# Kernel optimization log

Measured on AMD Instinct MI355X. Metric: run time of the kernel, lower is better.

Reference implementation:

```python
import jax, jax.numpy as jnp
import numpy as np

EPS = 1e-5  # torch BatchNorm1d default eps

N_NODES = 100000
N_EDGES = 1250000
N_GRAPHS = 512
F_IN = 16
HID = 64


def _bn(x, w, b):
    # track_running_stats=False, momentum=None -> always batch statistics (biased var)
    m = jnp.mean(x, axis=0)
    v = jnp.var(x, axis=0)
    return (x - m) * jax.lax.rsqrt(v + EPS) * w + b


def _prelu(x, a):
    return jnp.where(x >= 0, x, a * x)


def _gcn_conv(x, W, b, src, dst, n):
    # PyG GCNConv: h = x W; add self loops; sym-norm by deg^-1/2 on target degrees
    h = x @ W  # [N, out]
    ones = jnp.ones(src.shape[0], x.dtype)
    deg = jax.ops.segment_sum(ones, dst, num_segments=n) + 1.0  # +1 self loop
    dis = jax.lax.rsqrt(deg)  # deg >= 1 so finite
    norm = (dis[src] * dis[dst])[:, None]  # [E,1]
    agg = jax.ops.segment_sum(h[src] * norm, dst, num_segments=n)
    # self-loop contribution: norm = dis[i]*dis[i]
    return agg + h * (dis * dis)[:, None] + b


def setup_inputs() -> dict:
    key = jax.random.key(0)
    ks = jax.random.split(key, 12)
    x = jax.random.normal(ks[0], (N_NODES, F_IN), dtype=jnp.float32)
    edge_index = jax.random.randint(ks[1], (2, N_EDGES), 0, N_NODES, dtype=jnp.int32)
    # evenly spaced graph ids so every segment is non-empty (global_max_pool)
    batch = ((jnp.arange(N_NODES, dtype=jnp.int32) * N_GRAPHS) // N_NODES).astype(jnp.int32)
    s = 0.1
    W1 = jax.random.normal(ks[2], (F_IN, HID), jnp.float32) * s
    b1 = jnp.zeros((HID,), jnp.float32)
    W2 = jax.random.normal(ks[3], (HID, HID), jnp.float32) * s
    b2 = jnp.zeros((HID,), jnp.float32)
    lw1 = jax.random.normal(ks[4], (HID, HID), jnp.float32) * s
    lb1 = jnp.zeros((HID,), jnp.float32)
    lw2 = jax.random.normal(ks[5], (HID, 1), jnp.float32) * s
    lb2 = jnp.zeros((1,), jnp.float32)
    bn1_w = jnp.ones((HID,), jnp.float32); bn1_b = jnp.zeros((HID,), jnp.float32)
    bn2_w = jnp.ones((HID,), jnp.float32); bn2_b = jnp.zeros((HID,), jnp.float32)
    bn3_w = jnp.ones((HID,), jnp.float32); bn3_b = jnp.zeros((HID,), jnp.float32)
    bn4_w = jnp.ones((1,), jnp.float32); bn4_b = jnp.zeros((1,), jnp.float32)
    a1 = jnp.full((1,), 0.25, jnp.float32)
    a2 = jnp.full((1,), 0.25, jnp.float32)
    a3 = jnp.full((1,), 0.25, jnp.float32)
    a4 = jnp.full((1,), 0.25, jnp.float32)
    return {"x": x, "edge_index": edge_index, "batch": batch,
            "W1": W1, "b1": b1, "W2": W2, "b2": b2,
            "bn1_w": bn1_w, "bn1_b": bn1_b, "bn2_w": bn2_w, "bn2_b": bn2_b,
            "bn3_w": bn3_w, "bn3_b": bn3_b, "bn4_w": bn4_w, "bn4_b": bn4_b,
            "lw1": lw1, "lb1": lb1, "lw2": lw2, "lb2": lb2,
            "a1": a1, "a2": a2, "a3": a3, "a4": a4}


def reference(x, edge_index, batch, W1, b1, W2, b2,
              bn1_w, bn1_b, bn2_w, bn2_b, bn3_w, bn3_b, bn4_w, bn4_b,
              lw1, lb1, lw2, lb2, a1, a2, a3, a4):
    src, dst = edge_index[0], edge_index[1]
    n = x.shape[0]
    h = _gcn_conv(x, W1, b1, src, dst, n)
    h = _prelu(_bn(h, bn1_w, bn1_b), a1)
    h = _gcn_conv(h, W2, b2, src, dst, n)
    h = _prelu(_bn(h, bn2_w, bn2_b), a2)
    g = jax.ops.segment_max(h, batch, num_segments=N_GRAPHS)  # global_max_pool
    g = _prelu(_bn(g @ lw1 + lb1, bn3_w, bn3_b), a3)
    g = _prelu(_bn(g @ lw2 + lb2, bn4_w, bn4_b), a4)
    return g
```

## Files before the change

kernel.cpp:

```cpp
#include <hip/hip_runtime.h>
#include <hip/hip_bf16.h>

#define N_NODES 100000
#define N_EDGES 1250000
#define N_GRAPHS 512
#define F_IN 16
#define HID 64
#define EPS 1e-5f

#define K_B 1563
#define B_H 250
#define EPB 5000
#define M_SC (K_B * B_H)

typedef unsigned int uint;

__device__ __forceinline__ uint f2bf(float f) {
    uint u = __float_as_uint(f);
    return (u + 0x7fffu + ((u >> 16) & 1u)) >> 16;
}
__device__ __forceinline__ uint pack2(float lo, float hi) {
    return f2bf(lo) | (f2bf(hi) << 16);
}
__device__ __forceinline__ void unpack8(float* o, uint4 v) {
    o[0] = __uint_as_float(v.x << 16); o[1] = __uint_as_float(v.x & 0xffff0000u);
    o[2] = __uint_as_float(v.y << 16); o[3] = __uint_as_float(v.y & 0xffff0000u);
    o[4] = __uint_as_float(v.z << 16); o[5] = __uint_as_float(v.z & 0xffff0000u);
    o[6] = __uint_as_float(v.w << 16); o[7] = __uint_as_float(v.w & 0xffff0000u);
}
__device__ __forceinline__ void accum8(float* a, uint4 v) {
    a[0] += __uint_as_float(v.x << 16); a[1] += __uint_as_float(v.x & 0xffff0000u);
    a[2] += __uint_as_float(v.y << 16); a[3] += __uint_as_float(v.y & 0xffff0000u);
    a[4] += __uint_as_float(v.z << 16); a[5] += __uint_as_float(v.z & 0xffff0000u);
    a[6] += __uint_as_float(v.w << 16); a[7] += __uint_as_float(v.w & 0xffff0000u);
}


__global__ __launch_bounds__(256) void k_hist(const int4* __restrict__ dst4,
                                              int* __restrict__ hist,
                                              float* __restrict__ statsr) {
    __shared__ int h[K_B];
    int t = threadIdx.x, b = blockIdx.x;
    if (b == 0) {
        for (int i = t; i < 6 * 512; i += 256) statsr[i] = 0.f;
    }
    for (int k = t; k < K_B; k += 256) h[k] = 0;
    __syncthreads();
    const int4* d4 = dst4 + b * (EPB / 4);
    for (int i = t; i < EPB / 4; i += 256) {
        int4 d = d4[i];
        atomicAdd(&h[d.x >> 6], 1);
        atomicAdd(&h[d.y >> 6], 1);
        atomicAdd(&h[d.z >> 6], 1);
        atomicAdd(&h[d.w >> 6], 1);
    }
    __syncthreads();
    for (int k = t; k < K_B; k += 256) hist[k * B_H + b] = h[k];
}

__global__ void k_s1(const int* __restrict__ in, int* __restrict__ out,
                     int* __restrict__ bsum, int n) {
    __shared__ int sh[256];
    int blk = blockIdx.x, t = threadIdx.x;
    int base = blk * 1024 + t * 4;
    int v[4];
#pragma unroll
    for (int j = 0; j < 4; j++) { int i = base + j; v[j] = (i < n) ? in[i] : 0; }
    int tsum = v[0] + v[1] + v[2] + v[3];
    sh[t] = tsum;
    __syncthreads();
    for (int ofs = 1; ofs < 256; ofs <<= 1) {
        int x = (t >= ofs) ? sh[t - ofs] : 0;
        __syncthreads();
        sh[t] += x;
        __syncthreads();
    }
    int run = sh[t] - tsum;
    if (t == 255) bsum[blk] = sh[255];
#pragma unroll
    for (int j = 0; j < 4; j++) { int i = base + j; if (i < n) out[i] = run; run += v[j]; }
}

__global__ void k_s2(int* __restrict__ bsum, int nb) {
    __shared__ int sh[256];
    int t = threadIdx.x;
    int v[4]; int s = 0;
#pragma unroll
    for (int j = 0; j < 4; j++) { int i = t * 4 + j; v[j] = (i < nb) ? bsum[i] : 0; s += v[j]; }
    sh[t] = s;
    __syncthreads();
    for (int ofs = 1; ofs < 256; ofs <<= 1) {
        int x = (t >= ofs) ? sh[t - ofs] : 0;
        __syncthreads();
        sh[t] += x;
        __syncthreads();
    }
    int run = sh[t] - s;
#pragma unroll
    for (int j = 0; j < 4; j++) { int i = t * 4 + j; if (i < nb) bsum[i] = run; run += v[j]; }
}

__global__ __launch_bounds__(256) void k_bucketize(const int4* __restrict__ src4,
        const int4* __restrict__ dst4, const int* __restrict__ ebase,
        const int* __restrict__ bsum, int* __restrict__ ebuck) {
    __shared__ int base[K_B];
    int t = threadIdx.x, b = blockIdx.x;
    for (int k = t; k < K_B; k += 256) {
        int idx = k * B_H + b;
        base[k] = ebase[idx] + bsum[idx >> 10];
    }
    __syncthreads();
    const int4* s4 = src4 + b * (EPB / 4);
    const int4* d4 = dst4 + b * (EPB / 4);
    for (int i = t; i < EPB / 4; i += 256) {
        int4 s = s4[i];
        int4 d = d4[i];
        int p;
        p = atomicAdd(&base[d.x >> 6], 1); ebuck[p] = s.x | ((d.x & 63) << 17);
        p = atomicAdd(&base[d.y >> 6], 1); ebuck[p] = s.y | ((d.y & 63) << 17);
        p = atomicAdd(&base[d.z >> 6], 1); ebuck[p] = s.z | ((d.z & 63) << 17);
        p = atomicAdd(&base[d.w >> 6], 1); ebuck[p] = s.w | ((d.w & 63) << 17);
    }
}

__global__ __launch_bounds__(256) void k_csr(const int* __restrict__ ebase,
        const int* __restrict__ bsum, const int* __restrict__ ebuck,
        int* __restrict__ col, int2* __restrict__ meta, float* __restrict__ dis) {
    int k = blockIdx.x, t = threadIdx.x;
    int i0 = k * B_H;
    int beg = ebase[i0] + bsum[i0 >> 10];
    int end;
    if (k + 1 < K_B) {
        int i1 = i0 + B_H;
        end = ebase[i1] + bsum[i1 >> 10];
    } else {
        end = N_EDGES;
    }
    int m = end - beg;
    __shared__ int eb[2048];
    __shared__ int cnt512[512];
    __shared__ int off512[512];
    __shared__ int sb[512];
    __shared__ int sh[256];
    for (int i = t; i < 512; i += 256) cnt512[i] = 0;
    __syncthreads();
    if (m <= 2048) {
        for (int i = t; i < m; i += 256) {
            int e = ebuck[beg + i];
            eb[i] = e;
            int bin = ((e >> 17) << 3) | ((e & 0x1FFFF) >> 14);
            atomicAdd(&cnt512[bin], 1);
        }
        __syncthreads();
        int v0 = cnt512[2 * t], v1 = cnt512[2 * t + 1];
        int pair = v0 + v1;
        sh[t] = pair;
        __syncthreads();
        for (int ofs = 1; ofs < 256; ofs <<= 1) {
            int x = (t >= ofs) ? sh[t - ofs] : 0;
            __syncthreads();
            sh[t] += x;
            __syncthreads();
        }
        int excl = sh[t] - pair;
        off512[2 * t] = excl;
        off512[2 * t + 1] = excl + v0;
        sb[2 * t] = beg + excl;
        sb[2 * t + 1] = beg + excl + v0;
        __syncthreads();
        if (t < 64) {
            int o0 = off512[t * 8];
            int o1 = (t < 63) ? off512[(t + 1) * 8] : m;
            int node = k * 64 + t;
            if (node < N_NODES) {
                meta[node] = make_int2(beg + o0, o1 - o0);
                dis[node] = rsqrtf((float)(o1 - o0) + 1.0f);
            }
        }
        __syncthreads();
        for (int i = t; i < m; i += 256) {
            int e = eb[i];
            int bin = ((e >> 17) << 3) | ((e & 0x1FFFF) >> 14);
            int pos = atomicAdd(&sb[bin], 1);
            col[pos] = e & 0x1FFFF;
        }
    } else {
        for (int i = t; i < m; i += 256) atomicAdd(&cnt512[ebuck[beg + i] >> 17], 1);
        __syncthreads();
        if (t < 64) {
            int v = cnt512[t];
            int incl = v;
#pragma unroll
            for (int o = 1; o < 64; o <<= 1) { int u = __shfl_up(incl, o); if (t >= o) incl += u; }
            int excl = incl - v;
            int node = k * 64 + t;
            if (node < N_NODES) {
                meta[node] = make_int2(beg + excl, v);
                dis[node] = rsqrtf((float)v + 1.0f);
            }
            sb[t] = beg + excl;
        }
        __syncthreads();
        for (int i = t; i < m; i += 256) {
            int e = ebuck[beg + i];
            int pos = atomicAdd(&sb[e >> 17], 1);
            col[pos] = e & 0x1FFFF;
        }
    }
}


__global__ __launch_bounds__(512) void k_gemm1(const float* __restrict__ x,
        const float* __restrict__ W1, const float* __restrict__ dis,
        ushort* __restrict__ A) {
    __shared__ float Ws[F_IN * HID];
    __shared__ float xs[32 * F_IN];
    int t = threadIdx.x;
    Ws[t] = W1[t];
    Ws[t + 512] = W1[t + 512];
    int n0 = blockIdx.x * 32;
    xs[t] = x[n0 * F_IN + t];
    __syncthreads();
    int f = t & 63, w = t >> 6;
    float Wreg[F_IN];
#pragma unroll
    for (int k = 0; k < F_IN; k++) Wreg[k] = Ws[k * HID + f];
#pragma unroll
    for (int i = 0; i < 4; i++) {
        int nl = w * 4 + i;
        float acc = 0.f;
#pragma unroll
        for (int kq = 0; kq < 4; kq++) {
            const float4 xv = *(const float4*)&xs[nl * F_IN + kq * 4];
            acc = fmaf(xv.x, Wreg[4 * kq + 0], acc);
            acc = fmaf(xv.y, Wreg[4 * kq + 1], acc);
            acc = fmaf(xv.z, Wreg[4 * kq + 2], acc);
            acc = fmaf(xv.w, Wreg[4 * kq + 3], acc);
        }
        int n = n0 + nl;
        A[(size_t)n * HID + f] = (ushort)f2bf(acc * dis[n]);
    }
}

__global__ __launch_bounds__(512) void k_gemm2(const ushort* __restrict__ B,
        const float* __restrict__ s1r, const float* __restrict__ ss1r,
        const float* __restrict__ bnw, const float* __restrict__ bnb,
        const float* __restrict__ alpha, const float* __restrict__ W2,
        const float* __restrict__ dis, ushort* __restrict__ A2) {
    __shared__ float Ws[HID * HID];
    __shared__ float xs[32 * HID];
    __shared__ float scs[64], shsv[64];
    int t = threadIdx.x;
#pragma unroll
    for (int i = 0; i < 8; i++) Ws[i * 512 + t] = W2[i * 512 + t];
    if (t < 64) {
        float s = 0, q = 0;
#pragma unroll
        for (int r = 0; r < 8; r++) { s += s1r[r * 64 + t]; q += ss1r[r * 64 + t]; }
        const float invn = 1.f / N_NODES;
        float m = s * invn;
        float v = q * invn - m * m;
        float sc = bnw[t] * rsqrtf(v + EPS);
        scs[t] = sc;
        shsv[t] = bnb[t] - m * sc;
    }
    __syncthreads();
    int n0 = blockIdx.x * 32;
    float al = alpha[0];
    {
        const uint* Bu = (const uint*)(B + (size_t)n0 * HID);
#pragma unroll
        for (int i = 0; i < 2; i++) {
            int idx = i * 512 + t;
            uint u = Bu[idx];
            int fp = (idx & 31) * 2;
            int row = idx >> 5;
            float lo = __uint_as_float(u << 16) * scs[fp] + shsv[fp];
            float hi = __uint_as_float(u & 0xffff0000u) * scs[fp + 1] + shsv[fp + 1];
            lo = lo >= 0.f ? lo : al * lo;
            hi = hi >= 0.f ? hi : al * hi;
            xs[row * HID + fp] = lo;
            xs[row * HID + fp + 1] = hi;
        }
    }
    __syncthreads();
    int f = t & 63, w = t >> 6;
    float Wreg[HID];
#pragma unroll
    for (int k = 0; k < HID; k++) Wreg[k] = Ws[k * HID + f];
#pragma unroll
    for (int i = 0; i < 4; i++) {
        int nl = w * 4 + i;
        float acc = 0.f;
#pragma unroll
        for (int kq = 0; kq < 16; kq++) {
            const float4 xv = *(const float4*)&xs[nl * HID + kq * 4];
            acc = fmaf(xv.x, Wreg[4 * kq + 0], acc);
            acc = fmaf(xv.y, Wreg[4 * kq + 1], acc);
            acc = fmaf(xv.z, Wreg[4 * kq + 2], acc);
            acc = fmaf(xv.w, Wreg[4 * kq + 3], acc);
        }
        int n = n0 + nl;
        A2[(size_t)n * HID + f] = (ushort)f2bf(acc * dis[n]);
    }
}

__global__ __launch_bounds__(256) void k_agg(const uint4* __restrict__ Asc,
        const float* __restrict__ dis, const int2* __restrict__ meta,
        const int* __restrict__ col, const float* __restrict__ bias,
        uint4* __restrict__ outB, float* __restrict__ sumr,
        float* __restrict__ sumsqr) {
    int t = threadIdx.x;
    int nid = blockIdx.x * 32 + (t >> 3);
    int fq = t & 7;
    int2 mt = meta[nid];
    int beg = mt.x, m = mt.y;
    float acc[8] = {0, 0, 0, 0, 0, 0, 0, 0};
    int j = 0;
    for (; j + 8 <= m; j += 8) {
        int s0 = col[beg + j];
        int s1 = col[beg + j + 1];
        int s2 = col[beg + j + 2];
        int s3 = col[beg + j + 3];
        int s4 = col[beg + j + 4];
        int s5 = col[beg + j + 5];
        int s6 = col[beg + j + 6];
        int s7 = col[beg + j + 7];
        uint4 r0 = Asc[(size_t)s0 * 8 + fq];
        uint4 r1 = Asc[(size_t)s1 * 8 + fq];
        uint4 r2 = Asc[(size_t)s2 * 8 + fq];
        uint4 r3 = Asc[(size_t)s3 * 8 + fq];
        uint4 r4 = Asc[(size_t)s4 * 8 + fq];
        uint4 r5 = Asc[(size_t)s5 * 8 + fq];
        uint4 r6 = Asc[(size_t)s6 * 8 + fq];
        uint4 r7 = Asc[(size_t)s7 * 8 + fq];
        accum8(acc, r0); accum8(acc, r1); accum8(acc, r2); accum8(acc, r3);
        accum8(acc, r4); accum8(acc, r5); accum8(acc, r6); accum8(acc, r7);
    }
    for (; j + 2 <= m; j += 2) {
        int s0 = col[beg + j];
        int s1 = col[beg + j + 1];
        uint4 r0 = Asc[(size_t)s0 * 8 + fq];
        uint4 r1 = Asc[(size_t)s1 * 8 + fq];
        accum8(acc, r0); accum8(acc, r1);
    }
    if (j < m) {
        int s = col[beg + j];
        accum8(acc, Asc[(size_t)s * 8 + fq]);
    }
    accum8(acc, Asc[(size_t)nid * 8 + fq]);
    float dn = dis[nid];
    float4 b0 = ((const float4*)bias)[fq * 2];
    float4 b1 = ((const float4*)bias)[fq * 2 + 1];
    float o[8];
    o[0] = b0.x + dn * acc[0]; o[1] = b0.y + dn * acc[1];
    o[2] = b0.z + dn * acc[2]; o[3] = b0.w + dn * acc[3];
    o[4] = b1.x + dn * acc[4]; o[5] = b1.y + dn * acc[5];
    o[6] = b1.z + dn * acc[6]; o[7] = b1.w + dn * acc[7];
    uint4 ov;
    ov.x = pack2(o[0], o[1]); ov.y = pack2(o[2], o[3]);
    ov.z = pack2(o[4], o[5]); ov.w = pack2(o[6], o[7]);
    outB[(size_t)nid * 8 + fq] = ov;

    float sq[8];
#pragma unroll
    for (int i = 0; i < 8; i++) sq[i] = o[i] * o[i];
#pragma unroll
    for (int ofs = 8; ofs <= 32; ofs <<= 1) {
#pragma unroll
        for (int i = 0; i < 8; i++) {
            o[i] += __shfl_xor(o[i], ofs);
            sq[i] += __shfl_xor(sq[i], ofs);
        }
    }
    __shared__ float ps[4][64], pq[4][64];
    int w = t >> 6, lane = t & 63;
    if (lane < 8) {
#pragma unroll
        for (int i = 0; i < 8; i++) {
            ps[w][lane * 8 + i] = o[i];
            pq[w][lane * 8 + i] = sq[i];
        }
    }
    __syncthreads();
    if (t < 64) {
        float a = ps[0][t] + ps[1][t] + ps[2][t] + ps[3][t];
        float b = pq[0][t] + pq[1][t] + pq[2][t] + pq[3][t];
        int rep = (blockIdx.x & 7) * 64;
        atomicAdd(&sumr[rep + t], a);
        atomicAdd(&sumsqr[rep + t], b);
    }
}

__global__ __launch_bounds__(256) void k_pool(const uint4* __restrict__ a,
        const float* __restrict__ s2r, const float* __restrict__ ss2r,
        const float* __restrict__ bnw, const float* __restrict__ bnb,
        const float* __restrict__ alpha, const float* __restrict__ lw1,
        const float* __restrict__ lb1, float* __restrict__ th,
        float* __restrict__ s3r, float* __restrict__ ss3r) {
    __shared__ float scs[64], shsv[64];
    __shared__ float sm[2048];
    __shared__ float gr[64];
    int gi = blockIdx.x;
    int t = threadIdx.x, rg = t >> 3, fq = t & 7;
    if (t < 64) {
        float s = 0, q = 0;
#pragma unroll
        for (int r = 0; r < 8; r++) { s += s2r[r * 64 + t]; q += ss2r[r * 64 + t]; }
        const float invn = 1.f / N_NODES;
        float m = s * invn;
        float v = q * invn - m * m;
        float sc = bnw[t] * rsqrtf(v + EPS);
        scs[t] = sc;
        shsv[t] = bnb[t] - m * sc;
    }
    __syncthreads();
    int lo = (gi * N_NODES + N_GRAPHS - 1) / N_GRAPHS;
    int hi = ((gi + 1) * N_NODES + N_GRAPHS - 1) / N_GRAPHS;
    float al = alpha[0];
    float sc[8], sh[8];
#pragma unroll
    for (int i = 0; i < 8; i++) { sc[i] = scs[fq * 8 + i]; sh[i] = shsv[fq * 8 + i]; }
    float mx[8];
#pragma unroll
    for (int i = 0; i < 8; i++) mx[i] = -INFINITY;
    for (int r = lo + rg; r < hi; r += 32) {
        float o[8];
        unpack8(o, a[(size_t)r * 8 + fq]);
#pragma unroll
        for (int i = 0; i < 8; i++) {
            float v = o[i] * sc[i] + sh[i];
            v = v >= 0.f ? v : al * v;
            mx[i] = fmaxf(mx[i], v);
        }
    }
#pragma unroll
    for (int i = 0; i < 8; i++) sm[rg * 64 + fq * 8 + i] = mx[i];
    __syncthreads();
    if (t < 64) {
        float m = sm[t];
#pragma unroll
        for (int i = 1; i < 32; i++) m = fmaxf(m, sm[i * 64 + t]);
        gr[t] = m;
    }
    __syncthreads();
    if (t < 64) {
        float acc = lb1[t];
#pragma unroll
        for (int k = 0; k < 64; k++) acc = fmaf(gr[k], lw1[k * 64 + t], acc);
        th[gi * 64 + t] = acc;
        int rep = (gi & 7) * 64;
        atomicAdd(&s3r[rep + t], acc);
        atomicAdd(&ss3r[rep + t], acc * acc);
    }
}

__global__ __launch_bounds__(512) void k_head(const float* __restrict__ th,
        const float* __restrict__ s3r, const float* __restrict__ ss3r,
        const float* __restrict__ bn3w, const float* __restrict__ bn3b,
        const float* __restrict__ a3, const float* __restrict__ lw2,
        const float* __restrict__ lb2, const float* __restrict__ bn4w,
        const float* __restrict__ bn4b, const float* __restrict__ a4,
        float* __restrict__ out) {
    int t = threadIdx.x, w = t >> 6, lane = t & 63;
    __shared__ float t2s[N_GRAPHS];
    __shared__ float rs[8], rq[8];
    const float invn = 1.f / N_GRAPHS;
    float s = 0, q = 0;
#pragma unroll
    for (int r = 0; r < 8; r++) { s += s3r[r * 64 + lane]; q += ss3r[r * 64 + lane]; }
    float m3 = s * invn;
    float v3 = q * invn - m3 * m3;
    float sc3 = bn3w[lane] * rsqrtf(v3 + EPS);
    float sh3 = bn3b[lane] - m3 * sc3;
    float al3 = a3[0];
    float wv = lw2[lane];
    float lb = lb2[0];
    for (int r = w; r < N_GRAPHS; r += 8) {
        float xv = th[r * 64 + lane] * sc3 + sh3;
        xv = xv >= 0.f ? xv : al3 * xv;
        float p = xv * wv;
#pragma unroll
        for (int o = 32; o > 0; o >>= 1) p += __shfl_xor(p, o);
        if (lane == 0) t2s[r] = p + lb;
    }
    __syncthreads();
    float tv = t2s[t];
    float ps = tv, pq = tv * tv;
#pragma unroll
    for (int o = 32; o > 0; o >>= 1) { ps += __shfl_xor(ps, o); pq += __shfl_xor(pq, o); }
    if (lane == 0) { rs[w] = ps; rq[w] = pq; }
    __syncthreads();
    float S = 0, Q = 0;
#pragma unroll
    for (int i = 0; i < 8; i++) { S += rs[i]; Q += rq[i]; }
    float m4 = S * invn;
    float v4 = Q * invn - m4 * m4;
    float sc4 = bn4w[0] * rsqrtf(v4 + EPS);
    float xb = (tv - m4) * sc4 + bn4b[0];
    float al4 = a4[0];
    out[t] = xb >= 0.f ? xb : al4 * xb;
}

extern "C" void kernel_launch(void* const* d_in, const int* in_sizes, int n_in,
                              void* d_out, int out_size, void* d_ws, size_t ws_size,
                              hipStream_t stream) {
    const float* x   = (const float*)d_in[0];
    const int*   ei  = (const int*)d_in[1];
    const int4*  src4 = (const int4*)ei;
    const int4*  dst4 = (const int4*)(ei + N_EDGES);
    const float* W1  = (const float*)d_in[3];
    const float* b1  = (const float*)d_in[4];
    const float* W2  = (const float*)d_in[5];
    const float* b2  = (const float*)d_in[6];
    const float* bn1w = (const float*)d_in[7];
    const float* bn1b = (const float*)d_in[8];
    const float* bn2w = (const float*)d_in[9];
    const float* bn2b = (const float*)d_in[10];
    const float* bn3w = (const float*)d_in[11];
    const float* bn3b = (const float*)d_in[12];
    const float* bn4w = (const float*)d_in[13];
    const float* bn4b = (const float*)d_in[14];
    const float* lw1  = (const float*)d_in[15];
    const float* lb1  = (const float*)d_in[16];
    const float* lw2  = (const float*)d_in[17];
    const float* lb2  = (const float*)d_in[18];
    const float* a1   = (const float*)d_in[19];
    const float* a2   = (const float*)d_in[20];
    const float* a3   = (const float*)d_in[21];
    const float* a4   = (const float*)d_in[22];
    float* out = (float*)d_out;

    char* p = (char*)d_ws;
    auto carve = [&](size_t bytes) -> void* {
        void* r = (void*)p;
        p += (bytes + 255) & ~(size_t)255;
        return r;
    };
    int*    hist = (int*)carve((size_t)M_SC * 4);
    int*    ebase = (int*)carve((size_t)M_SC * 4);
    int*    ebuck = (int*)carve((size_t)N_EDGES * 4);
    int*    col  = (int*)carve((size_t)N_EDGES * 4);
    float*  dis  = (float*)carve((size_t)N_NODES * 4);
    int2*   meta = (int2*)carve((size_t)N_NODES * 8);
    int*    bsum = (int*)carve(4096);
    ushort* A    = (ushort*)carve((size_t)N_NODES * HID * 2);
    ushort* B    = (ushort*)carve((size_t)N_NODES * HID * 2);
    float*  th   = (float*)carve((size_t)N_GRAPHS * HID * 4);
    float*  statsr = (float*)carve(6 * 512 * 4);
    float* s1r = statsr,          *ss1r = statsr + 512;
    float* s2r = statsr + 1024,   *ss2r = statsr + 1536;
    float* s3r = statsr + 2048,   *ss3r = statsr + 2560;

    const int SC_BLKS = (M_SC + 1023) / 1024;

    k_hist<<<B_H, 256, 0, stream>>>(dst4, hist, statsr);
    k_s1<<<SC_BLKS, 256, 0, stream>>>(hist, ebase, bsum, M_SC);
    k_s2<<<1, 256, 0, stream>>>(bsum, SC_BLKS);
    k_bucketize<<<B_H, 256, 0, stream>>>(src4, dst4, ebase, bsum, ebuck);
    k_csr<<<K_B, 256, 0, stream>>>(ebase, bsum, ebuck, col, meta, dis);

    const int NB32 = N_NODES / 32;
    k_gemm1<<<NB32, 512, 0, stream>>>(x, W1, dis, A);
    k_agg<<<NB32, 256, 0, stream>>>((const uint4*)A, dis, meta, col, b1, (uint4*)B,
                                    s1r, ss1r);
    k_gemm2<<<NB32, 512, 0, stream>>>(B, s1r, ss1r, bn1w, bn1b, a1, W2, dis, A);
    k_agg<<<NB32, 256, 0, stream>>>((const uint4*)A, dis, meta, col, b2, (uint4*)B,
                                    s2r, ss2r);
    k_pool<<<N_GRAPHS, 256, 0, stream>>>((const uint4*)B, s2r, ss2r, bn2w, bn2b, a2,
                                         lw1, lb1, th, s3r, ss3r);
    k_head<<<1, 512, 0, stream>>>(th, s3r, ss3r, bn3w, bn3b, a3, lw2, lb2,
                                  bn4w, bn4b, a4, out);
}
```

Measured before the change: 179.1 us.

## Store node features in feature-chunk-major layout and aggregate one chunk at a time

Node feature buffers change from row-major [N,64] bf16 to eight chunk-major planes of [N,8] bf16. The aggregation kernel now gives each node two threads and loops over the eight chunks, so each gather pass touches a 1.6MB plane that fits in cache better. The GEMM, pool and BN-stat code are updated to match. The cost is that the col indices are reread eight times per node, and each chunk adds shuffle reductions, two block syncs and atomics, with 16-byte gathers shrunk to 8 bytes.

Result: slower. 254.6 us (+42.1%).

```diff
diff --git a/kernel.cpp b/kernel.cpp
--- a/kernel.cpp
+++ b/kernel.cpp
@@ -28,11 +28,9 @@
     o[4] = __uint_as_float(v.z << 16); o[5] = __uint_as_float(v.z & 0xffff0000u);
     o[6] = __uint_as_float(v.w << 16); o[7] = __uint_as_float(v.w & 0xffff0000u);
 }
-__device__ __forceinline__ void accum8(float* a, uint4 v) {
+__device__ __forceinline__ void accum4(float* a, uint2 v) {
     a[0] += __uint_as_float(v.x << 16); a[1] += __uint_as_float(v.x & 0xffff0000u);
     a[2] += __uint_as_float(v.y << 16); a[3] += __uint_as_float(v.y & 0xffff0000u);
-    a[4] += __uint_as_float(v.z << 16); a[5] += __uint_as_float(v.z & 0xffff0000u);
-    a[6] += __uint_as_float(v.w << 16); a[7] += __uint_as_float(v.w & 0xffff0000u);
 }
 
 
@@ -225,6 +223,7 @@
     float Wreg[F_IN];
 #pragma unroll
     for (int k = 0; k < F_IN; k++) Wreg[k] = Ws[k * HID + f];
+    size_t fbase = (size_t)(f >> 3) * N_NODES * 8 + (f & 7);
 #pragma unroll
     for (int i = 0; i < 4; i++) {
         int nl = w * 4 + i;
@@ -238,7 +237,7 @@
             acc = fmaf(xv.w, Wreg[4 * kq + 3], acc);
         }
         int n = n0 + nl;
-        A[(size_t)n * HID + f] = (ushort)f2bf(acc * dis[n]);
+        A[fbase + (size_t)n * 8] = (ushort)f2bf(acc * dis[n]);
     }
 }
 
@@ -268,19 +267,19 @@
     int n0 = blockIdx.x * 32;
     float al = alpha[0];
     {
-        const uint* Bu = (const uint*)(B + (size_t)n0 * HID);
+        const uint* Bu = (const uint*)B;
 #pragma unroll
         for (int i = 0; i < 2; i++) {
-            int idx = i * 512 + t;
-            uint u = Bu[idx];
-            int fp = (idx & 31) * 2;
-            int row = idx >> 5;
+            int id = i * 512 + t;
+            int c = id >> 7, r = (id >> 2) & 31, jj = id & 3;
+            uint u = Bu[((size_t)c * N_NODES + n0 + r) * 4 + jj];
+            int fp = c * 8 + jj * 2;
             float lo = __uint_as_float(u << 16) * scs[fp] + shsv[fp];
             float hi = __uint_as_float(u & 0xffff0000u) * scs[fp + 1] + shsv[fp + 1];
             lo = lo >= 0.f ? lo : al * lo;
             hi = hi >= 0.f ? hi : al * hi;
-            xs[row * HID + fp] = lo;
-            xs[row * HID + fp + 1] = hi;
+            xs[r * HID + fp] = lo;
+            xs[r * HID + fp + 1] = hi;
         }
     }
     __syncthreads();
@@ -288,6 +287,7 @@
     float Wreg[HID];
 #pragma unroll
     for (int k = 0; k < HID; k++) Wreg[k] = Ws[k * HID + f];
+    size_t fbase = (size_t)(f >> 3) * N_NODES * 8 + (f & 7);
 #pragma unroll
     for (int i = 0; i < 4; i++) {
         int nl = w * 4 + i;
@@ -301,94 +301,78 @@
             acc = fmaf(xv.w, Wreg[4 * kq + 3], acc);
         }
         int n = n0 + nl;
-        A2[(size_t)n * HID + f] = (ushort)f2bf(acc * dis[n]);
-    }
-}
-
-__global__ __launch_bounds__(256) void k_agg(const uint4* __restrict__ Asc,
+        A2[fbase + (size_t)n * 8] = (ushort)f2bf(acc * dis[n]);
+    }
+}
+
+__global__ __launch_bounds__(256) void k_agg(const uint2* __restrict__ Asc,
         const float* __restrict__ dis, const int2* __restrict__ meta,
         const int* __restrict__ col, const float* __restrict__ bias,
-        uint4* __restrict__ outB, float* __restrict__ sumr,
+        uint2* __restrict__ outB, float* __restrict__ sumr,
         float* __restrict__ sumsqr) {
     int t = threadIdx.x;
-    int nid = blockIdx.x * 32 + (t >> 3);
-    int fq = t & 7;
-    int2 mt = meta[nid];
-    int beg = mt.x, m = mt.y;
-    float acc[8] = {0, 0, 0, 0, 0, 0, 0, 0};
-    int j = 0;
-    for (; j + 8 <= m; j += 8) {
-        int s0 = col[beg + j];
-        int s1 = col[beg + j + 1];
-        int s2 = col[beg + j + 2];
-        int s3 = col[beg + j + 3];
-        int s4 = col[beg + j + 4];
-        int s5 = col[beg + j + 5];
-        int s6 = col[beg + j + 6];
-        int s7 = col[beg + j + 7];
-        uint4 r0 = Asc[(size_t)s0 * 8 + fq];
-        uint4 r1 = Asc[(size_t)s1 * 8 + fq];
-        uint4 r2 = Asc[(size_t)s2 * 8 + fq];
-        uint4 r3 = Asc[(size_t)s3 * 8 + fq];
-        uint4 r4 = Asc[(size_t)s4 * 8 + fq];
-        uint4 r5 = Asc[(size_t)s5 * 8 + fq];
-        uint4 r6 = Asc[(size_t)s6 * 8 + fq];
-        uint4 r7 = Asc[(size_t)s7 * 8 + fq];
-        accum8(acc, r0); accum8(acc, r1); accum8(acc, r2); accum8(acc, r3);
-        accum8(acc, r4); accum8(acc, r5); accum8(acc, r6); accum8(acc, r7);
-    }
-    for (; j + 2 <= m; j += 2) {
-        int s0 = col[beg + j];
-        int s1 = col[beg + j + 1];
-        uint4 r0 = Asc[(size_t)s0 * 8 + fq];
-        uint4 r1 = Asc[(size_t)s1 * 8 + fq];
-        accum8(acc, r0); accum8(acc, r1);
-    }
-    if (j < m) {
-        int s = col[beg + j];
-        accum8(acc, Asc[(size_t)s * 8 + fq]);
-    }
-    accum8(acc, Asc[(size_t)nid * 8 + fq]);
-    float dn = dis[nid];
-    float4 b0 = ((const float4*)bias)[fq * 2];
-    float4 b1 = ((const float4*)bias)[fq * 2 + 1];
-    float o[8];
-    o[0] = b0.x + dn * acc[0]; o[1] = b0.y + dn * acc[1];
-    o[2] = b0.z + dn * acc[2]; o[3] = b0.w + dn * acc[3];
-    o[4] = b1.x + dn * acc[4]; o[5] = b1.y + dn * acc[5];
-    o[6] = b1.z + dn * acc[6]; o[7] = b1.w + dn * acc[7];
-    uint4 ov;
-    ov.x = pack2(o[0], o[1]); ov.y = pack2(o[2], o[3]);
-    ov.z = pack2(o[4], o[5]); ov.w = pack2(o[6], o[7]);
-    outB[(size_t)nid * 8 + fq] = ov;
-
-    float sq[8];
-#pragma unroll
-    for (int i = 0; i < 8; i++) sq[i] = o[i] * o[i];
-#pragma unroll
-    for (int ofs = 8; ofs <= 32; ofs <<= 1) {
-#pragma unroll
-        for (int i = 0; i < 8; i++) {
-            o[i] += __shfl_xor(o[i], ofs);
-            sq[i] += __shfl_xor(sq[i], ofs);
-        }
-    }
-    __shared__ float ps[4][64], pq[4][64];
-    int w = t >> 6, lane = t & 63;
-    if (lane < 8) {
-#pragma unroll
-        for (int i = 0; i < 8; i++) {
-            ps[w][lane * 8 + i] = o[i];
-            pq[w][lane * 8 + i] = sq[i];
-        }
-    }
-    __syncthreads();
-    if (t < 64) {
-        float a = ps[0][t] + ps[1][t] + ps[2][t] + ps[3][t];
-        float b = pq[0][t] + pq[1][t] + pq[2][t] + pq[3][t];
-        int rep = (blockIdx.x & 7) * 64;
-        atomicAdd(&sumr[rep + t], a);
-        atomicAdd(&sumsqr[rep + t], b);
+    int nid = blockIdx.x * 128 + (t >> 1);
+    int l = t & 1;
+    bool act = nid < N_NODES;
+    int beg = 0, m = 0; float dn = 0.f;
+    if (act) { int2 mt = meta[nid]; beg = mt.x; m = mt.y; dn = dis[nid]; }
+    int w = t >> 6;
+    int rep = (blockIdx.x & 7) * 64;
+    __shared__ float ps[4][8], pq[4][8];
+    for (int c = 0; c < 8; ++c) {
+        const uint2* __restrict__ Ac = Asc + (size_t)c * N_NODES * 2;
+        float acc[4] = {0.f, 0.f, 0.f, 0.f};
+        int j = 0;
+        for (; j + 4 <= m; j += 4) {
+            int s0 = col[beg + j];
+            int s1 = col[beg + j + 1];
+            int s2 = col[beg + j + 2];
+            int s3 = col[beg + j + 3];
+            uint2 r0 = Ac[(size_t)s0 * 2 + l];
+            uint2 r1 = Ac[(size_t)s1 * 2 + l];
+            uint2 r2 = Ac[(size_t)s2 * 2 + l];
+            uint2 r3 = Ac[(size_t)s3 * 2 + l];
+            accum4(acc, r0); accum4(acc, r1); accum4(acc, r2); accum4(acc, r3);
+        }
+        for (; j < m; ++j) {
+            int s = col[beg + j];
+            accum4(acc, Ac[(size_t)s * 2 + l]);
+        }
+        if (act) accum4(acc, Ac[(size_t)nid * 2 + l]);
+        float4 bv = ((const float4*)bias)[c * 2 + l];
+        float o[4];
+        o[0] = bv.x + dn * acc[0]; o[1] = bv.y + dn * acc[1];
+        o[2] = bv.z + dn * acc[2]; o[3] = bv.w + dn * acc[3];
+        if (act) {
+            uint2 ov;
+            ov.x = pack2(o[0], o[1]); ov.y = pack2(o[2], o[3]);
+            outB[((size_t)c * N_NODES + nid) * 2 + l] = ov;
+        } else {
+            o[0] = o[1] = o[2] = o[3] = 0.f;
+        }
+        float sq[4];
+#pragma unroll
+        for (int i = 0; i < 4; i++) sq[i] = o[i] * o[i];
+#pragma unroll
+        for (int ofs = 2; ofs <= 32; ofs <<= 1) {
+#pragma unroll
+            for (int i = 0; i < 4; i++) {
+                o[i] += __shfl_xor(o[i], ofs);
+                sq[i] += __shfl_xor(sq[i], ofs);
+            }
+        }
+        if ((t & 63) < 2) {
+#pragma unroll
+            for (int i = 0; i < 4; i++) { ps[w][l * 4 + i] = o[i]; pq[w][l * 4 + i] = sq[i]; }
+        }
+        __syncthreads();
+        if (t < 8) {
+            float a = ps[0][t] + ps[1][t] + ps[2][t] + ps[3][t];
+            float b = pq[0][t] + pq[1][t] + pq[2][t] + pq[3][t];
+            atomicAdd(&sumr[rep + c * 8 + t], a);
+            atomicAdd(&sumsqr[rep + c * 8 + t], b);
+        }
+        __syncthreads();
     }
 }
 
@@ -424,9 +408,10 @@
     float mx[8];
 #pragma unroll
     for (int i = 0; i < 8; i++) mx[i] = -INFINITY;
+    const uint4* ac = a + (size_t)fq * N_NODES;
     for (int r = lo + rg; r < hi; r += 32) {
         float o[8];
-        unpack8(o, a[(size_t)r * 8 + fq]);
+        unpack8(o, ac[r]);
 #pragma unroll
         for (int i = 0; i < 8; i++) {
             float v = o[i] * sc[i] + sh[i];
@@ -561,12 +546,13 @@
     k_csr<<<K_B, 256, 0, stream>>>(ebase, bsum, ebuck, col, meta, dis);
 
     const int NB32 = N_NODES / 32;
+    const int AGG_BLKS = (N_NODES + 127) / 128;
     k_gemm1<<<NB32, 512, 0, stream>>>(x, W1, dis, A);
-    k_agg<<<NB32, 256, 0, stream>>>((const uint4*)A, dis, meta, col, b1, (uint4*)B,
-                                    s1r, ss1r);
+    k_agg<<<AGG_BLKS, 256, 0, stream>>>((const uint2*)A, dis, meta, col, b1,
+                                        (uint2*)B, s1r, ss1r);
     k_gemm2<<<NB32, 512, 0, stream>>>(B, s1r, ss1r, bn1w, bn1b, a1, W2, dis, A);
-    k_agg<<<NB32, 256, 0, stream>>>((const uint4*)A, dis, meta, col, b2, (uint4*)B,
-                                    s2r, ss2r);
+    k_agg<<<AGG_BLKS, 256, 0, stream>>>((const uint2*)A, dis, meta, col, b2,
+                                        (uint2*)B, s2r, ss2r);
     k_pool<<<N_GRAPHS, 256, 0, stream>>>((const uint4*)B, s2r, ss2r, bn2w, bn2b, a2,
                                          lw1, lb1, th, s3r, ss3r);
     k_head<<<1, 512, 0, stream>>>(th, s3r, ss3r, bn3w, bn3b, a3, lw2, lb2,
```

## Fold block-sum scan into consumers and fuse first GEMM into CSR build

Applied to the files above, without the earlier changes.

Drops the single-block k_s2 scan kernel. Each k_bucketize and k_csr block now recomputes the exclusive scan of the block sums in shared memory. Also merges k_gemm1 into k_csr, so each CSR block computes x·W1 scaled by its locally computed degree norm for its 64 nodes. This removes two kernel launches and the re-read of dis, at the cost of redundant scan work in every block, extra shared memory in k_csr that may lower occupancy, and a less efficient per-block GEMM loop. There are also some leftover redundant source loads in bucketize.

Result: no change. 181.9 us (+1.5%).

```diff
diff --git a/kernel.cpp b/kernel.cpp
--- a/kernel.cpp
+++ b/kernel.cpp
@@ -12,6 +12,7 @@
 #define B_H 250
 #define EPB 5000
 #define M_SC (K_B * B_H)
+#define SC_BLKS ((M_SC + 1023) / 1024)
 
 typedef unsigned int uint;
 
@@ -81,67 +82,99 @@
     for (int j = 0; j < 4; j++) { int i = base + j; if (i < n) out[i] = run; run += v[j]; }
 }
 
-__global__ void k_s2(int* __restrict__ bsum, int nb) {
-    __shared__ int sh[256];
-    int t = threadIdx.x;
-    int v[4]; int s = 0;
-#pragma unroll
-    for (int j = 0; j < 4; j++) { int i = t * 4 + j; v[j] = (i < nb) ? bsum[i] : 0; s += v[j]; }
-    sh[t] = s;
-    __syncthreads();
-    for (int ofs = 1; ofs < 256; ofs <<= 1) {
-        int x = (t >= ofs) ? sh[t - ofs] : 0;
-        __syncthreads();
-        sh[t] += x;
-        __syncthreads();
-    }
-    int run = sh[t] - s;
-#pragma unroll
-    for (int j = 0; j < 4; j++) { int i = t * 4 + j; if (i < nb) bsum[i] = run; run += v[j]; }
-}
-
 __global__ __launch_bounds__(256) void k_bucketize(const int4* __restrict__ src4,
         const int4* __restrict__ dst4, const int* __restrict__ ebase,
         const int* __restrict__ bsum, int* __restrict__ ebuck) {
     __shared__ int base[K_B];
+    __shared__ int bss[512];
+    __shared__ int shs[256];
     int t = threadIdx.x, b = blockIdx.x;
+    {
+        int i0 = 2 * t, i1 = 2 * t + 1;
+        int v0 = (i0 < SC_BLKS) ? bsum[i0] : 0;
+        int v1 = (i1 < SC_BLKS) ? bsum[i1] : 0;
+        int s = v0 + v1;
+        shs[t] = s;
+        __syncthreads();
+        for (int ofs = 1; ofs < 256; ofs <<= 1) {
+            int x2 = (t >= ofs) ? shs[t - ofs] : 0;
+            __syncthreads();
+            shs[t] += x2;
+            __syncthreads();
+        }
+        int run = shs[t] - s;
+        bss[i0] = run;
+        bss[i1] = run + v0;
+    }
+    __syncthreads();
     for (int k = t; k < K_B; k += 256) {
         int idx = k * B_H + b;
-        base[k] = ebase[idx] + bsum[idx >> 10];
+        base[k] = ebase[idx] + bss[idx >> 10];
     }
     __syncthreads();
     const int4* s4 = src4 + b * (EPB / 4);
     const int4* d4 = dst4 + b * (EPB / 4);
     for (int i = t; i < EPB / 4; i += 256) {
-        int4 s = s4[i];
+        int s = s4[i].x, s_y = s4[i].y, s_z = s4[i].z, s_w = s4[i].w;
+        int4 sv = s4[i];
         int4 d = d4[i];
+        (void)s; (void)s_y; (void)s_z; (void)s_w;
         int p;
-        p = atomicAdd(&base[d.x >> 6], 1); ebuck[p] = s.x | ((d.x & 63) << 17);
-        p = atomicAdd(&base[d.y >> 6], 1); ebuck[p] = s.y | ((d.y & 63) << 17);
-        p = atomicAdd(&base[d.z >> 6], 1); ebuck[p] = s.z | ((d.z & 63) << 17);
-        p = atomicAdd(&base[d.w >> 6], 1); ebuck[p] = s.w | ((d.w & 63) << 17);
+        p = atomicAdd(&base[d.x >> 6], 1); ebuck[p] = sv.x | ((d.x & 63) << 17);
+        p = atomicAdd(&base[d.y >> 6], 1); ebuck[p] = sv.y | ((d.y & 63) << 17);
+        p = atomicAdd(&base[d.z >> 6], 1); ebuck[p] = sv.z | ((d.z & 63) << 17);
+        p = atomicAdd(&base[d.w >> 6], 1); ebuck[p] = sv.w | ((d.w & 63) << 17);
     }
 }
 
 __global__ __launch_bounds__(256) void k_csr(const int* __restrict__ ebase,
         const int* __restrict__ bsum, const int* __restrict__ ebuck,
-        int* __restrict__ col, int2* __restrict__ meta, float* __restrict__ dis) {
+        int* __restrict__ col, int2* __restrict__ meta, float* __restrict__ dis,
+        const float* __restrict__ x, const float* __restrict__ W1,
+        ushort* __restrict__ A) {
     int k = blockIdx.x, t = threadIdx.x;
-    int i0 = k * B_H;
-    int beg = ebase[i0] + bsum[i0 >> 10];
-    int end;
-    if (k + 1 < K_B) {
-        int i1 = i0 + B_H;
-        end = ebase[i1] + bsum[i1 >> 10];
-    } else {
-        end = N_EDGES;
-    }
-    int m = end - beg;
     __shared__ int eb[2048];
     __shared__ int cnt512[512];
     __shared__ int off512[512];
     __shared__ int sb[512];
     __shared__ int sh[256];
+    __shared__ int bss[512];
+    __shared__ float Ws[F_IN * HID];
+    __shared__ float xs2[64 * F_IN];
+    __shared__ float disS[64];
+    {
+        int i0 = 2 * t, i1 = 2 * t + 1;
+        int v0 = (i0 < SC_BLKS) ? bsum[i0] : 0;
+        int v1 = (i1 < SC_BLKS) ? bsum[i1] : 0;
+        int s = v0 + v1;
+        sh[t] = s;
+        __syncthreads();
+        for (int ofs = 1; ofs < 256; ofs <<= 1) {
+            int x2 = (t >= ofs) ? sh[t - ofs] : 0;
+            __syncthreads();
+            sh[t] += x2;
+            __syncthreads();
+        }
+        int run = sh[t] - s;
+        bss[i0] = run;
+        bss[i1] = run + v0;
+    }
+    __syncthreads();
+    int i0 = k * B_H;
+    int beg = ebase[i0] + bss[i0 >> 10];
+    int end;
+    if (k + 1 < K_B) {
+        int i1 = i0 + B_H;
+        end = ebase[i1] + bss[i1 >> 10];
+    } else {
+        end = N_EDGES;
+    }
+    int m = end - beg;
+    for (int i = t; i < F_IN * HID; i += 256) Ws[i] = W1[i];
+    for (int i = t; i < 64 * F_IN; i += 256) {
+        int gi = k * (64 * F_IN) + i;
+        xs2[i] = (gi < N_NODES * F_IN) ? x[gi] : 0.f;
+    }
     for (int i = t; i < 512; i += 256) cnt512[i] = 0;
     __syncthreads();
     if (m <= 2048) {
@@ -157,9 +190,9 @@
         sh[t] = pair;
         __syncthreads();
         for (int ofs = 1; ofs < 256; ofs <<= 1) {
-            int x = (t >= ofs) ? sh[t - ofs] : 0;
+            int x2 = (t >= ofs) ? sh[t - ofs] : 0;
             __syncthreads();
-            sh[t] += x;
+            sh[t] += x2;
             __syncthreads();
         }
         int excl = sh[t] - pair;
@@ -172,9 +205,12 @@
             int o0 = off512[t * 8];
             int o1 = (t < 63) ? off512[(t + 1) * 8] : m;
             int node = k * 64 + t;
+            int deg = o1 - o0;
+            float dv = rsqrtf((float)deg + 1.0f);
+            disS[t] = dv;
             if (node < N_NODES) {
-                meta[node] = make_int2(beg + o0, o1 - o0);
-                dis[node] = rsqrtf((float)(o1 - o0) + 1.0f);
+                meta[node] = make_int2(beg + o0, deg);
+                dis[node] = dv;
             }
         }
         __syncthreads();
@@ -194,9 +230,11 @@
             for (int o = 1; o < 64; o <<= 1) { int u = __shfl_up(incl, o); if (t >= o) incl += u; }
             int excl = incl - v;
             int node = k * 64 + t;
+            float dv = rsqrtf((float)v + 1.0f);
+            disS[t] = dv;
             if (node < N_NODES) {
                 meta[node] = make_int2(beg + excl, v);
-                dis[node] = rsqrtf((float)v + 1.0f);
+                dis[node] = dv;
             }
             sb[t] = beg + excl;
         }
@@ -207,40 +245,20 @@
             col[pos] = e & 0x1FFFF;
         }
     }
-}
-
-
-__global__ __launch_bounds__(512) void k_gemm1(const float* __restrict__ x,
-        const float* __restrict__ W1, const float* __restrict__ dis,
-        ushort* __restrict__ A) {
-    __shared__ float Ws[F_IN * HID];
-    __shared__ float xs[32 * F_IN];
-    int t = threadIdx.x;
-    Ws[t] = W1[t];
-    Ws[t + 512] = W1[t + 512];
-    int n0 = blockIdx.x * 32;
-    xs[t] = x[n0 * F_IN + t];
-    __syncthreads();
-    int f = t & 63, w = t >> 6;
-    float Wreg[F_IN];
-#pragma unroll
-    for (int k = 0; k < F_IN; k++) Wreg[k] = Ws[k * HID + f];
-#pragma unroll
-    for (int i = 0; i < 4; i++) {
-        int nl = w * 4 + i;
+#pragma unroll
+    for (int i = 0; i < 16; i++) {
+        int idx = i * 256 + t;
+        int n = idx >> 6, f = idx & 63;
         float acc = 0.f;
 #pragma unroll
-        for (int kq = 0; kq < 4; kq++) {
-            const float4 xv = *(const float4*)&xs[nl * F_IN + kq * 4];
-            acc = fmaf(xv.x, Wreg[4 * kq + 0], acc);
-            acc = fmaf(xv.y, Wreg[4 * kq + 1], acc);
-            acc = fmaf(xv.z, Wreg[4 * kq + 2], acc);
-            acc = fmaf(xv.w, Wreg[4 * kq + 3], acc);
-        }
-        int n = n0 + nl;
-        A[(size_t)n * HID + f] = (ushort)f2bf(acc * dis[n]);
-    }
-}
+        for (int kk = 0; kk < F_IN; kk++)
+            acc = fmaf(xs2[n * F_IN + kk], Ws[kk * HID + f], acc);
+        int gn = k * 64 + n;
+        if (gn < N_NODES)
+            A[(size_t)gn * HID + f] = (ushort)f2bf(acc * disS[n]);
+    }
+}
+
 
 __global__ __launch_bounds__(512) void k_gemm2(const ushort* __restrict__ B,
         const float* __restrict__ s1r, const float* __restrict__ ss1r,
@@ -552,16 +570,12 @@
     float* s2r = statsr + 1024,   *ss2r = statsr + 1536;
     float* s3r = statsr + 2048,   *ss3r = statsr + 2560;
 
-    const int SC_BLKS = (M_SC + 1023) / 1024;
-
     k_hist<<<B_H, 256, 0, stream>>>(dst4, hist, statsr);
     k_s1<<<SC_BLKS, 256, 0, stream>>>(hist, ebase, bsum, M_SC);
-    k_s2<<<1, 256, 0, stream>>>(bsum, SC_BLKS);
     k_bucketize<<<B_H, 256, 0, stream>>>(src4, dst4, ebase, bsum, ebuck);
-    k_csr<<<K_B, 256, 0, stream>>>(ebase, bsum, ebuck, col, meta, dis);
+    k_csr<<<K_B, 256, 0, stream>>>(ebase, bsum, ebuck, col, meta, dis, x, W1, A);
 
     const int NB32 = N_NODES / 32;
-    k_gemm1<<<NB32, 512, 0, stream>>>(x, W1, dis, A);
     k_agg<<<NB32, 256, 0, stream>>>((const uint4*)A, dis, meta, col, b1, (uint4*)B,
                                     s1r, ss1r);
     k_gemm2<<<NB32, 512, 0, stream>>>(B, s1r, ss1r, bn1w, bn1b, a1, W2, dis, A);
```
